# Performance work log

Measured on AMD Instinct MI355X. Metric: run time of the kernel, lower is better.

The kernel has to match this reference:

```python
import jax, jax.numpy as jnp
import numpy as np

N, D, W, S = 16384, 256, 64, 8  # utterances, embed dim, attention half-window, speakers


def setup_inputs() -> dict:
    key = jax.random.key(0)
    ks = jax.random.split(key, 8)
    scale = 1.0 / np.sqrt(D)
    return {
        "x": jax.random.normal(ks[0], (N, D), jnp.float32),
        "speaker_ids": jax.random.randint(ks[1], (N,), 0, S, jnp.int32),
        "W_att": jax.random.normal(ks[2], (D, D), jnp.float32) * scale,
        "W_pred": jax.random.normal(ks[3], (D, D), jnp.float32) * scale,
        "W_suc": jax.random.normal(ks[4], (D, D), jnp.float32) * scale,
        "W_same": jax.random.normal(ks[5], (D, D), jnp.float32) * scale,
        "W_diff": jax.random.normal(ks[6], (D, D), jnp.float32) * scale,
    }


def reference(x, speaker_ids, W_att, W_pred, W_suc, W_same, W_diff):
    n = x.shape[0]
    pad = jnp.zeros((W, D), x.dtype)
    # windowed gather: for utterance i, neighbors at offsets [-W, W-1] (2W slots)
    win_idx = jnp.arange(n)[:, None] + jnp.arange(2 * W)[None, :]  # index into padded [N+2W]
    xp = jnp.concatenate([pad, x, pad], axis=0)                    # [N+2W, D]
    windows = xp[win_idx]                                          # [N, 2W, D]
    # raw_attn[i,w] = (edge_att_weights(windows[i,w])) . x[i]
    raw_attn = jnp.einsum("nwd,ed,ne->nw", windows, W_att, x)      # [N, 2W]
    attn = jax.nn.softmax(raw_attn, axis=1)
    # relation masks over the band: j = i + offset
    offs = jnp.arange(2 * W) - W                                   # [-W, W-1]
    j = jnp.arange(n)[:, None] + offs[None, :]                     # [N, 2W]
    valid = (j >= 0) & (j < n)
    jc = jnp.clip(j, 0, n - 1)
    same_spk = speaker_ids[jc] == speaker_ids[:, None]
    masks = [
        valid & (offs >= 0)[None, :],   # pred: edges to current/future within window
        valid & (offs < 0)[None, :],    # suc: edges to past within window
        valid & same_spk,               # same speaker within window
        valid & ~same_spk,              # different speaker within window
    ]
    # relation-specific GCN aggregation: h = sum_r A_r @ (x @ W_r), A_r banded
    h = jnp.zeros_like(x)
    for Wr, m in zip([W_pred, W_suc, W_same, W_diff], masks):
        support = x @ Wr                                           # [N, D]
        sp = jnp.concatenate([pad, support, pad], axis=0)[win_idx]  # [N, 2W, D]
        h = h + jnp.einsum("nw,nwd->nd", attn * m, sp)
    return jax.nn.log_softmax(h, axis=1)
```

## Files before the change

### kernel.cpp

```cpp
#include <hip/hip_runtime.h>
#include <hip/hip_bf16.h>

typedef unsigned short u16;
typedef unsigned int u32;
typedef __attribute__((ext_vector_type(8))) short short8;
typedef __attribute__((ext_vector_type(4))) float floatx4;

#define NU 16384
#define DIM 256

#define XHo 0u
#define XLo 4194304u
#define XRo 8388608u
#define YHo 12582912u
#define YLo 16777216u
#define ST0 20971520u
#define STROW 16512u
#define STMAT 4227072u
#define WH0o 33652736u
#define WL0o 33718272u
#define WRo  33783808u

__device__ __forceinline__ u16 bfh(float v) {
  return (u16)(__float_as_uint(v) >> 16);
}
__device__ __forceinline__ float bup(u16 u) {
  return __uint_as_float(((u32)u) << 16);
}
__device__ __forceinline__ u16 bfrn(float v) {
  u32 u = __float_as_uint(v);
  return (u16)((u + 0x7fffu + ((u >> 16) & 1u)) >> 16);
}

__global__ __launch_bounds__(256) void xprep(const float* __restrict__ x,
                                             u16* __restrict__ ws) {
  int idx = (blockIdx.x * 256 + threadIdx.x) * 4;
  float4 v = *(const float4*)(x + idx);
  float a[4] = {v.x, v.y, v.z, v.w};
  u16 h[4], l[4], r[4];
#pragma unroll
  for (int q = 0; q < 4; ++q) {
    h[q] = bfh(a[q]);
    l[q] = bfh(a[q] - bup(h[q]));
    r[q] = bfrn(a[q]);
  }
  *(ushort4*)(ws + XHo + idx) = make_ushort4(h[0], h[1], h[2], h[3]);
  *(ushort4*)(ws + XLo + idx) = make_ushort4(l[0], l[1], l[2], l[3]);
  *(ushort4*)(ws + XRo + idx) = make_ushort4(r[0], r[1], r[2], r[3]);
}

__global__ __launch_bounds__(256) void wprep(
    const float* __restrict__ wat, const float* __restrict__ wpr,
    const float* __restrict__ wsu, const float* __restrict__ wsm,
    const float* __restrict__ wdf, u16* __restrict__ ws) {
  const int s = blockIdx.x, mat = blockIdx.y, n = threadIdx.x;
  const float* Wa = (mat == 0) ? wat : (mat == 1) ? wpr : (mat == 2) ? wsm : wsu;
  const float* Wb = (mat == 0) ? wat : (mat == 1) ? wsu : (mat == 2) ? wdf : wdf;
  const float c1  = (mat == 0) ? 0.f : (mat == 3) ? 1.f : -1.f;
  u16 hbuf[32], lbuf[32];
#pragma unroll 8
  for (int k = 0; k < 32; ++k) {
    float v = Wa[(s * 32 + k) * 256 + n] + c1 * Wb[(s * 32 + k) * 256 + n];
    if (mat == 0) { hbuf[k] = bfh(v); lbuf[k] = bfh(v - bup(hbuf[k])); }
    else          { hbuf[k] = bfrn(v); }
  }
  u16* dh = ws + ((mat == 0) ? WH0o : (WRo + (size_t)(mat - 1) * 65536))
             + (size_t)s * 8192 + n * 32;
#pragma unroll
  for (int p = 0; p < 4; ++p) *(uint4*)(dh + p * 8) = ((const uint4*)hbuf)[p];
  if (mat == 0) {
    u16* dl = ws + WL0o + (size_t)s * 8192 + n * 32;
#pragma unroll
    for (int p = 0; p < 4; ++p) *(uint4*)(dl + p * 8) = ((const uint4*)lbuf)[p];
  }
}

__global__ __launch_bounds__(256) void gzero(u16* __restrict__ ws) {
  int g = blockIdx.x * 256 + threadIdx.x;
  int r = g >> 13, rem = g & 8191;
  int d = rem >> 5, p = rem & 31;
  size_t base = ST0 + (size_t)r * STMAT + (size_t)d * STROW;
  size_t off = (p < 16) ? (base + p * 4) : (base + 16448 + (p - 16) * 4);
  *(ushort4*)(ws + off) = make_ushort4(0, 0, 0, 0);
}

__global__ __launch_bounds__(512) void gemmS(u16* __restrict__ ws) {
  __shared__ __align__(16) u16 Ahs[2048], Als[2048];
  __shared__ __align__(16) u16 BU[20480];

  const int t = threadIdx.x, mat = blockIdx.y, row0 = blockIdx.x * 64;
  const int w = t >> 6, ln = t & 15, quad = (t & 63) >> 4, q8 = quad * 8;
  const int n2base = w * 32;

  const u16* Wh = ws + ((mat == 0) ? WH0o : (WRo + (size_t)(mat - 1) * 65536));
  const u16* Wl = ws + WL0o;
  const u16* xh = ws + XHo;
  const u16* xl = ws + XLo;
  const u16* xr = ws + XRo;

  floatx4 acc[4][2];
#pragma unroll
  for (int m = 0; m < 4; ++m)
#pragma unroll
    for (int n2 = 0; n2 < 2; ++n2) acc[m][n2] = (floatx4){0.f, 0.f, 0.f, 0.f};

  for (int s = 0; s < 8; ++s) {
    if (mat == 0) {
      int c = t & 255, arow = c >> 2, apart = (c & 3) * 8;
      const u16* src = ((t < 256) ? xh : xl) + (size_t)(row0 + arow) * 256 + s * 32 + apart;
      u16* dst = ((t < 256) ? Ahs : Als) + arow * 32 + apart;
      *(uint4*)dst = *(const uint4*)src;
    } else if (t < 256) {
      int arow = t >> 2, apart = (t & 3) * 8;
      *(uint4*)(Ahs + arow * 32 + apart) =
          *(const uint4*)(xr + (size_t)(row0 + arow) * 256 + s * 32 + apart);
    }
    if (mat == 0) {
#pragma unroll
      for (int cc = 0; cc < 4; ++cc) {
        int c = t + 512 * cc;
        const u16* src = ((c < 1024) ? Wh : Wl) + (size_t)s * 8192 + (c & 1023) * 8;
        u16* dst = ((c < 1024) ? BU : BU + 8192) + (c & 1023) * 8;
        *(uint4*)dst = *(const uint4*)src;
      }
    } else {
#pragma unroll
      for (int cc = 0; cc < 2; ++cc) {
        int c = t + 512 * cc;
        *(uint4*)(BU + c * 8) = *(const uint4*)(Wh + (size_t)s * 8192 + c * 8);
      }
    }
    __syncthreads();

    short8 ah[4], al[4];
#pragma unroll
    for (int m = 0; m < 4; ++m) {
      ah[m] = *(const short8*)(Ahs + (m * 16 + ln) * 32 + q8);
      if (mat == 0) al[m] = *(const short8*)(Als + (m * 16 + ln) * 32 + q8);
    }
    short8 bh[2], bl[2];
#pragma unroll
    for (int n2 = 0; n2 < 2; ++n2) {
      int n = n2base + n2 * 16 + ln;
      bh[n2] = *(const short8*)(BU + n * 32 + q8);
      if (mat == 0) bl[n2] = *(const short8*)(BU + 8192 + n * 32 + q8);
    }
#pragma unroll
    for (int m = 0; m < 4; ++m)
#pragma unroll
      for (int n2 = 0; n2 < 2; ++n2) {
        acc[m][n2] = __builtin_amdgcn_mfma_f32_16x16x32_bf16(ah[m], bh[n2], acc[m][n2], 0, 0, 0);
        if (mat == 0) {
          acc[m][n2] = __builtin_amdgcn_mfma_f32_16x16x32_bf16(ah[m], bl[n2], acc[m][n2], 0, 0, 0);
          acc[m][n2] = __builtin_amdgcn_mfma_f32_16x16x32_bf16(al[m], bh[n2], acc[m][n2], 0, 0, 0);
        }
      }
    __syncthreads();
  }

  if (mat == 0) {
#pragma unroll
    for (int m = 0; m < 4; ++m)
#pragma unroll
      for (int n2 = 0; n2 < 2; ++n2) {
        int col = n2base + n2 * 16 + ln;
#pragma unroll
        for (int r = 0; r < 4; ++r) {
          int row = row0 + m * 16 + quad * 4 + r;
          float y = acc[m][n2][r];
          u16 hh = bfh(y);
          ws[YHo + (size_t)row * 256 + col] = hh;
          ws[YLo + (size_t)row * 256 + col] = bfh(y - bup(hh));
        }
      }
  } else {
#pragma unroll
    for (int m = 0; m < 4; ++m)
#pragma unroll
      for (int n2 = 0; n2 < 2; ++n2) {
        int col = n2base + n2 * 16 + ln;
        ushort4 pk = make_ushort4(bfrn(acc[m][n2][0]), bfrn(acc[m][n2][1]),
                                  bfrn(acc[m][n2][2]), bfrn(acc[m][n2][3]));
        *(ushort4*)(BU + col * 80 + m * 16 + quad * 4) = pk;
      }
    __syncthreads();
    u16* STm = ws + ST0 + (size_t)(mat - 1) * STMAT;
#pragma unroll
    for (int cc = 0; cc < 4; ++cc) {
      int c = t + 512 * cc;
      int d = c >> 3, part = c & 7;
      *(uint4*)(STm + (size_t)d * STROW + 64 + row0 + part * 8) =
          *(const uint4*)(BU + d * 80 + part * 8);
    }
  }
}

__global__ __launch_bounds__(512) void fused_attn(
    const u16* __restrict__ ws, const int* __restrict__ spk,
    float* __restrict__ out)
{
  __shared__ float Plds[64][196];
  __shared__ __align__(16) u16 stg[30720];
  __shared__ int spkw[192];
  __shared__ float pmax[64][8], psum[64][8], gmaxs[64], glse[64];

  const int t    = threadIdx.x;
  const int w    = t >> 6;
  const int ln   = t & 15;
  const int quad = (t & 63) >> 4;
  const int q8   = quad * 8;
  const int i0   = blockIdx.x * 64;

  if (t < 192) {
    int j = i0 + t - 64;
    spkw[t] = spk[min(max(j, 0), NU - 1)];
  }

  floatx4 accP[6];
#pragma unroll
  for (int cc = 0; cc < 6; ++cc) accP[cc] = (floatx4){0.f, 0.f, 0.f, 0.f};
  const int m0  = (w >> 1) * 16;
  const int ct0 = (w & 1) * 6;

  for (int kd = 0; kd < DIM; kd += 32) {
#pragma unroll
    for (int cc = 0; cc < 4; ++cc) {
      int c = t + 512 * cc;
      if (c < 1536) {
        int row = c >> 3, sub = c & 7, hil = sub >> 2, part = sub & 3;
        int jc = min(max(i0 + row - 64, 0), NU - 1);
        const u16* src = ws + (hil ? XLo : XHo) + (size_t)jc * 256 + kd + part * 8;
        *(uint4*)(stg + (hil ? 6144 : 0) + row * 32 + part * 8) = *(const uint4*)src;
      } else {
        int c2 = c - 1536;
        int row = c2 >> 3, sub = c2 & 7, hil = sub >> 2, part = sub & 3;
        const u16* src = ws + (hil ? YLo : YHo) + (size_t)(i0 + row) * 256 + kd + part * 8;
        *(uint4*)(stg + 12288 + (hil ? 2048 : 0) + row * 32 + part * 8) = *(const uint4*)src;
      }
    }
    __syncthreads();

    short8 ah = *(const short8*)(stg + 12288 + (m0 + ln) * 32 + q8);
    short8 al = *(const short8*)(stg + 14336 + (m0 + ln) * 32 + q8);
#pragma unroll
    for (int cc = 0; cc < 6; ++cc) {
      int xrow = (ct0 + cc) * 16 + ln;
      short8 bh = *(const short8*)(stg + xrow * 32 + q8);
      short8 bl = *(const short8*)(stg + 6144 + xrow * 32 + q8);
      accP[cc] = __builtin_amdgcn_mfma_f32_16x16x32_bf16(ah, bh, accP[cc], 0, 0, 0);
      accP[cc] = __builtin_amdgcn_mfma_f32_16x16x32_bf16(ah, bl, accP[cc], 0, 0, 0);
      accP[cc] = __builtin_amdgcn_mfma_f32_16x16x32_bf16(al, bh, accP[cc], 0, 0, 0);
    }
    __syncthreads();
  }
#pragma unroll
  for (int cc = 0; cc < 6; ++cc)
#pragma unroll
    for (int r = 0; r < 4; ++r)
      Plds[m0 + quad * 4 + r][(ct0 + cc) * 16 + ln] = accP[cc][r];
  __syncthreads();

  {
    int row = t >> 3, s = t & 7;
    float vals[16];
    float mx = -3.4e38f;
#pragma unroll
    for (int q = 0; q < 16; ++q) {
      int c = row + s * 16 + q;
      int j = i0 + c - 64;
      float pv = ((j >= 0) && (j < NU)) ? Plds[row][c] : 0.f;
      vals[q] = pv;
      mx = fmaxf(mx, pv);
    }
#pragma unroll
    for (int o = 1; o < 8; o <<= 1) mx = fmaxf(mx, __shfl_xor(mx, o));
    float sm = 0.f;
#pragma unroll
    for (int q = 0; q < 16; ++q) { vals[q] = __expf(vals[q] - mx); sm += vals[q]; }
#pragma unroll
    for (int o = 1; o < 8; o <<= 1) sm += __shfl_xor(sm, o);
    float inv = 1.f / sm;
#pragma unroll
    for (int q = 0; q < 16; ++q) {
      int c = row + s * 16 + q;
      int j = i0 + c - 64;
      Plds[row][c] = ((j >= 0) && (j < NU)) ? vals[q] * inv : 0.f;
    }
#pragma unroll
    for (int q = 0; q < 8; ++q) {
      int c2 = row + 128 + s * 8 + q;
      if (c2 >= 192) c2 -= 192;
      Plds[row][c2] = 0.f;
    }
  }
  __syncthreads();

  const int n0 = w * 32;
  floatx4 acc2[4][2];
#pragma unroll
  for (int m = 0; m < 4; ++m)
#pragma unroll
    for (int n2 = 0; n2 < 2; ++n2) acc2[m][n2] = (floatx4){0.f, 0.f, 0.f, 0.f};

  for (int kj = 0; kj < 192; kj += 32) {
    const int jcol = i0 + kj;
#pragma unroll
    for (int cc = 0; cc < 6; ++cc) {
      int c = t + 512 * cc;
      int r = c >> 10, d = (c >> 2) & 255, part = c & 3;
      const u16* src = ws + ST0 + (size_t)r * STMAT + (size_t)d * STROW + jcol + part * 8;
      *(uint4*)(stg + r * 8192 + d * 32 + part * 8) = *(const uint4*)src;
    }
    {
      int row = t >> 3, cg = t & 7, cb = kj + cg * 4;
      float4 av = *(const float4*)(&Plds[row][cb]);
      float aa[4] = {av.x, av.y, av.z, av.w};
      int sr = spkw[row + 64];
      u16 b0[4], b1[4], b2[4];
#pragma unroll
      for (int q = 0; q < 4; ++q) {
        int c = cb + q;
        u16 ab = bfrn(aa[q]);
        b0[q] = (c - row >= 64) ? ab : (u16)0;
        b1[q] = (spkw[c] == sr) ? ab : (u16)0;
        b2[q] = ab;
      }
      *(ushort4*)(stg + 24576 + row * 32 + cg * 4) = make_ushort4(b0[0], b0[1], b0[2], b0[3]);
      *(ushort4*)(stg + 26624 + row * 32 + cg * 4) = make_ushort4(b1[0], b1[1], b1[2], b1[3]);
      *(ushort4*)(stg + 28672 + row * 32 + cg * 4) = make_ushort4(b2[0], b2[1], b2[2], b2[3]);
    }
    __syncthreads();

    short8 af[3][4], bfv[3][2];
#pragma unroll
    for (int r = 0; r < 3; ++r) {
#pragma unroll
      for (int m = 0; m < 4; ++m)
        af[r][m] = *(const short8*)(stg + 24576 + r * 2048 + (m * 16 + ln) * 32 + q8);
#pragma unroll
      for (int n2 = 0; n2 < 2; ++n2) {
        int d = n0 + n2 * 16 + ln;
        bfv[r][n2] = *(const short8*)(stg + r * 8192 + d * 32 + q8);
      }
    }
#pragma unroll
    for (int r = 0; r < 3; ++r)
#pragma unroll
      for (int m = 0; m < 4; ++m)
#pragma unroll
        for (int n2 = 0; n2 < 2; ++n2)
          acc2[m][n2] = __builtin_amdgcn_mfma_f32_16x16x32_bf16(
              af[r][m], bfv[r][n2], acc2[m][n2], 0, 0, 0);
    __syncthreads();
  }

#pragma unroll
  for (int m = 0; m < 4; ++m)
#pragma unroll
    for (int r = 0; r < 4; ++r) {
      float v = fmaxf(acc2[m][0][r], acc2[m][1][r]);
#pragma unroll
      for (int o = 1; o < 16; o <<= 1) v = fmaxf(v, __shfl_xor(v, o));
      if (ln == 0) pmax[m * 16 + quad * 4 + r][w] = v;
    }
  __syncthreads();
  if (t < 64) {
    float g = pmax[t][0];
#pragma unroll
    for (int ww = 1; ww < 8; ++ww) g = fmaxf(g, pmax[t][ww]);
    gmaxs[t] = g;
  }
  __syncthreads();
#pragma unroll
  for (int m = 0; m < 4; ++m)
#pragma unroll
    for (int r = 0; r < 4; ++r) {
      float g = gmaxs[m * 16 + quad * 4 + r];
      float e = __expf(acc2[m][0][r] - g) + __expf(acc2[m][1][r] - g);
#pragma unroll
      for (int o = 1; o < 16; o <<= 1) e += __shfl_xor(e, o);
      if (ln == 0) psum[m * 16 + quad * 4 + r][w] = e;
    }
  __syncthreads();
  if (t < 64) {
    float s = psum[t][0];
#pragma unroll
    for (int ww = 1; ww < 8; ++ww) s += psum[t][ww];
    glse[t] = gmaxs[t] + logf(s);
  }
  __syncthreads();

#pragma unroll
  for (int m = 0; m < 4; ++m) {
    int rl0 = m * 16 + quad * 4;
#pragma unroll
    for (int r = 0; r < 4; ++r) {
      float l = glse[rl0 + r];
      size_t rowg = (size_t)(i0 + rl0 + r) * DIM;
      out[rowg + n0 + ln]      = acc2[m][0][r] - l;
      out[rowg + n0 + 16 + ln] = acc2[m][1][r] - l;
    }
  }
}

extern "C" void kernel_launch(void* const* d_in, const int* in_sizes, int n_in,
                              void* d_out, int out_size, void* d_ws, size_t ws_size,
                              hipStream_t stream) {
  const float* x   = (const float*)d_in[0];
  const int*   spk = (const int*)d_in[1];
  const float* wat = (const float*)d_in[2];
  const float* wpr = (const float*)d_in[3];
  const float* wsu = (const float*)d_in[4];
  const float* wsm = (const float*)d_in[5];
  const float* wdf = (const float*)d_in[6];
  float* out = (float*)d_out;
  u16* ws = (u16*)d_ws;

  hipLaunchKernelGGL(xprep, dim3(4096), dim3(256), 0, stream, x, ws);
  hipLaunchKernelGGL(wprep, dim3(8, 4), dim3(256), 0, stream,
                     wat, wpr, wsu, wsm, wdf, ws);
  hipLaunchKernelGGL(gzero, dim3(96), dim3(256), 0, stream, ws);
  hipLaunchKernelGGL(gemmS, dim3(256, 4), dim3(512), 0, stream, ws);
  hipLaunchKernelGGL(fused_attn, dim3(256), dim3(512), 0, stream, ws, spk, out);
}
```

Baseline: 169.0 us.

## Fuse attention projection into attn kernel and shrink tiles to 32 rows

Moves the x@W_att projection (three-pass split-bf16) out of gemmS and into fused_attn, so Y stays in LDS instead of round-tripping through global memory. The attention tile drops from 64 to 32 rows with a 160-column window, giving 512 blocks of 256 threads, and the X and ST operands are read straight from global memory instead of being staged through LDS. The weight-prep and zero-fill kernels are merged into one launch. In exchange, each block recomputes its own projection and depends on cache hits for the global reads that used to be staged.

```diff
diff --git a/kernel.cpp b/kernel.cpp
--- a/kernel.cpp
+++ b/kernel.cpp
@@ -8,18 +8,19 @@
 
 #define NU 16384
 #define DIM 256
+#define WIN 160
+#define YST 264
+#define AST 168
 
 #define XHo 0u
 #define XLo 4194304u
 #define XRo 8388608u
-#define YHo 12582912u
-#define YLo 16777216u
-#define ST0 20971520u
+#define ST0 12582912u
 #define STROW 16512u
 #define STMAT 4227072u
-#define WH0o 33652736u
-#define WL0o 33718272u
-#define WRo  33783808u
+#define WH0o 25264128u
+#define WL0o 25329664u
+#define WRo  25395200u
 
 __device__ __forceinline__ u16 bfh(float v) {
   return (u16)(__float_as_uint(v) >> 16);
@@ -49,53 +50,50 @@
   *(ushort4*)(ws + XRo + idx) = make_ushort4(r[0], r[1], r[2], r[3]);
 }
 
-__global__ __launch_bounds__(256) void wprep(
+__global__ __launch_bounds__(256) void wpgz(
     const float* __restrict__ wat, const float* __restrict__ wpr,
     const float* __restrict__ wsu, const float* __restrict__ wsm,
     const float* __restrict__ wdf, u16* __restrict__ ws) {
-  const int s = blockIdx.x, mat = blockIdx.y, n = threadIdx.x;
-  const float* Wa = (mat == 0) ? wat : (mat == 1) ? wpr : (mat == 2) ? wsm : wsu;
-  const float* Wb = (mat == 0) ? wat : (mat == 1) ? wsu : (mat == 2) ? wdf : wdf;
-  const float c1  = (mat == 0) ? 0.f : (mat == 3) ? 1.f : -1.f;
-  u16 hbuf[32], lbuf[32];
+  const int b = blockIdx.x, t = threadIdx.x;
+  if (b < 32) {
+    const int s = b & 7, mat = b >> 3, n = t;
+    const float* Wa = (mat == 0) ? wat : (mat == 1) ? wpr : (mat == 2) ? wsm : wsu;
+    const float* Wb = (mat == 0) ? wat : (mat == 1) ? wsu : (mat == 2) ? wdf : wdf;
+    const float c1  = (mat == 0) ? 0.f : (mat == 3) ? 1.f : -1.f;
+    u16 hbuf[32], lbuf[32];
 #pragma unroll 8
-  for (int k = 0; k < 32; ++k) {
-    float v = Wa[(s * 32 + k) * 256 + n] + c1 * Wb[(s * 32 + k) * 256 + n];
-    if (mat == 0) { hbuf[k] = bfh(v); lbuf[k] = bfh(v - bup(hbuf[k])); }
-    else          { hbuf[k] = bfrn(v); }
-  }
-  u16* dh = ws + ((mat == 0) ? WH0o : (WRo + (size_t)(mat - 1) * 65536))
-             + (size_t)s * 8192 + n * 32;
-#pragma unroll
-  for (int p = 0; p < 4; ++p) *(uint4*)(dh + p * 8) = ((const uint4*)hbuf)[p];
-  if (mat == 0) {
-    u16* dl = ws + WL0o + (size_t)s * 8192 + n * 32;
-#pragma unroll
-    for (int p = 0; p < 4; ++p) *(uint4*)(dl + p * 8) = ((const uint4*)lbuf)[p];
-  }
-}
-
-__global__ __launch_bounds__(256) void gzero(u16* __restrict__ ws) {
-  int g = blockIdx.x * 256 + threadIdx.x;
-  int r = g >> 13, rem = g & 8191;
-  int d = rem >> 5, p = rem & 31;
-  size_t base = ST0 + (size_t)r * STMAT + (size_t)d * STROW;
-  size_t off = (p < 16) ? (base + p * 4) : (base + 16448 + (p - 16) * 4);
-  *(ushort4*)(ws + off) = make_ushort4(0, 0, 0, 0);
+    for (int k = 0; k < 32; ++k) {
+      float v = Wa[(s * 32 + k) * 256 + n] + c1 * Wb[(s * 32 + k) * 256 + n];
+      if (mat == 0) { hbuf[k] = bfh(v); lbuf[k] = bfh(v - bup(hbuf[k])); }
+      else          { hbuf[k] = bfrn(v); }
+    }
+    u16* dh = ws + ((mat == 0) ? WH0o : (WRo + (size_t)(mat - 1) * 65536))
+               + (size_t)s * 8192 + n * 32;
+#pragma unroll
+    for (int p = 0; p < 4; ++p) *(uint4*)(dh + p * 8) = ((const uint4*)hbuf)[p];
+    if (mat == 0) {
+      u16* dl = ws + WL0o + (size_t)s * 8192 + n * 32;
+#pragma unroll
+      for (int p = 0; p < 4; ++p) *(uint4*)(dl + p * 8) = ((const uint4*)lbuf)[p];
+    }
+  } else {
+    int g = (b - 32) * 256 + t;
+    int r = g >> 13, rem = g & 8191;
+    int d = rem >> 5, p = rem & 31;
+    size_t base = ST0 + (size_t)r * STMAT + (size_t)d * STROW;
+    size_t off = (p < 16) ? (base + p * 4) : (base + 16448 + (p - 16) * 4);
+    *(ushort4*)(ws + off) = make_ushort4(0, 0, 0, 0);
+  }
 }
 
 __global__ __launch_bounds__(512) void gemmS(u16* __restrict__ ws) {
-  __shared__ __align__(16) u16 Ahs[2048], Als[2048];
+  __shared__ __align__(16) u16 Ahs[2048];
   __shared__ __align__(16) u16 BU[20480];
 
-  const int t = threadIdx.x, mat = blockIdx.y, row0 = blockIdx.x * 64;
+  const int t = threadIdx.x, row0 = blockIdx.x * 64;
   const int w = t >> 6, ln = t & 15, quad = (t & 63) >> 4, q8 = quad * 8;
   const int n2base = w * 32;
-
-  const u16* Wh = ws + ((mat == 0) ? WH0o : (WRo + (size_t)(mat - 1) * 65536));
-  const u16* Wl = ws + WL0o;
-  const u16* xh = ws + XHo;
-  const u16* xl = ws + XLo;
+  const u16* Wh = ws + WRo + (size_t)blockIdx.y * 65536;
   const u16* xr = ws + XRo;
 
   floatx4 acc[4][2];
@@ -105,302 +103,273 @@
     for (int n2 = 0; n2 < 2; ++n2) acc[m][n2] = (floatx4){0.f, 0.f, 0.f, 0.f};
 
   for (int s = 0; s < 8; ++s) {
-    if (mat == 0) {
-      int c = t & 255, arow = c >> 2, apart = (c & 3) * 8;
-      const u16* src = ((t < 256) ? xh : xl) + (size_t)(row0 + arow) * 256 + s * 32 + apart;
-      u16* dst = ((t < 256) ? Ahs : Als) + arow * 32 + apart;
-      *(uint4*)dst = *(const uint4*)src;
-    } else if (t < 256) {
+    if (t < 256) {
       int arow = t >> 2, apart = (t & 3) * 8;
       *(uint4*)(Ahs + arow * 32 + apart) =
           *(const uint4*)(xr + (size_t)(row0 + arow) * 256 + s * 32 + apart);
     }
-    if (mat == 0) {
-#pragma unroll
-      for (int cc = 0; cc < 4; ++cc) {
-        int c = t + 512 * cc;
-        const u16* src = ((c < 1024) ? Wh : Wl) + (size_t)s * 8192 + (c & 1023) * 8;
-        u16* dst = ((c < 1024) ? BU : BU + 8192) + (c & 1023) * 8;
-        *(uint4*)dst = *(const uint4*)src;
-      }
-    } else {
-#pragma unroll
-      for (int cc = 0; cc < 2; ++cc) {
-        int c = t + 512 * cc;
-        *(uint4*)(BU + c * 8) = *(const uint4*)(Wh + (size_t)s * 8192 + c * 8);
-      }
+#pragma unroll
+    for (int cc = 0; cc < 2; ++cc) {
+      int c = t + 512 * cc;
+      *(uint4*)(BU + c * 8) = *(const uint4*)(Wh + (size_t)s * 8192 + c * 8);
     }
     __syncthreads();
 
-    short8 ah[4], al[4];
-#pragma unroll
-    for (int m = 0; m < 4; ++m) {
+    short8 ah[4];
+#pragma unroll
+    for (int m = 0; m < 4; ++m)
       ah[m] = *(const short8*)(Ahs + (m * 16 + ln) * 32 + q8);
-      if (mat == 0) al[m] = *(const short8*)(Als + (m * 16 + ln) * 32 + q8);
-    }
-    short8 bh[2], bl[2];
+    short8 bh[2];
+#pragma unroll
+    for (int n2 = 0; n2 < 2; ++n2)
+      bh[n2] = *(const short8*)(BU + (n2base + n2 * 16 + ln) * 32 + q8);
+#pragma unroll
+    for (int m = 0; m < 4; ++m)
+#pragma unroll
+      for (int n2 = 0; n2 < 2; ++n2)
+        acc[m][n2] = __builtin_amdgcn_mfma_f32_16x16x32_bf16(ah[m], bh[n2], acc[m][n2], 0, 0, 0);
+    __syncthreads();
+  }
+
+#pragma unroll
+  for (int m = 0; m < 4; ++m)
 #pragma unroll
     for (int n2 = 0; n2 < 2; ++n2) {
-      int n = n2base + n2 * 16 + ln;
-      bh[n2] = *(const short8*)(BU + n * 32 + q8);
-      if (mat == 0) bl[n2] = *(const short8*)(BU + 8192 + n * 32 + q8);
-    }
-#pragma unroll
-    for (int m = 0; m < 4; ++m)
-#pragma unroll
-      for (int n2 = 0; n2 < 2; ++n2) {
-        acc[m][n2] = __builtin_amdgcn_mfma_f32_16x16x32_bf16(ah[m], bh[n2], acc[m][n2], 0, 0, 0);
-        if (mat == 0) {
-          acc[m][n2] = __builtin_amdgcn_mfma_f32_16x16x32_bf16(ah[m], bl[n2], acc[m][n2], 0, 0, 0);
-          acc[m][n2] = __builtin_amdgcn_mfma_f32_16x16x32_bf16(al[m], bh[n2], acc[m][n2], 0, 0, 0);
-        }
-      }
-    __syncthreads();
-  }
-
-  if (mat == 0) {
-#pragma unroll
-    for (int m = 0; m < 4; ++m)
-#pragma unroll
-      for (int n2 = 0; n2 < 2; ++n2) {
-        int col = n2base + n2 * 16 + ln;
-#pragma unroll
-        for (int r = 0; r < 4; ++r) {
-          int row = row0 + m * 16 + quad * 4 + r;
-          float y = acc[m][n2][r];
-          u16 hh = bfh(y);
-          ws[YHo + (size_t)row * 256 + col] = hh;
-          ws[YLo + (size_t)row * 256 + col] = bfh(y - bup(hh));
-        }
-      }
-  } else {
-#pragma unroll
-    for (int m = 0; m < 4; ++m)
-#pragma unroll
-      for (int n2 = 0; n2 < 2; ++n2) {
-        int col = n2base + n2 * 16 + ln;
-        ushort4 pk = make_ushort4(bfrn(acc[m][n2][0]), bfrn(acc[m][n2][1]),
-                                  bfrn(acc[m][n2][2]), bfrn(acc[m][n2][3]));
-        *(ushort4*)(BU + col * 80 + m * 16 + quad * 4) = pk;
-      }
-    __syncthreads();
-    u16* STm = ws + ST0 + (size_t)(mat - 1) * STMAT;
-#pragma unroll
-    for (int cc = 0; cc < 4; ++cc) {
-      int c = t + 512 * cc;
-      int d = c >> 3, part = c & 7;
-      *(uint4*)(STm + (size_t)d * STROW + 64 + row0 + part * 8) =
-          *(const uint4*)(BU + d * 80 + part * 8);
-    }
-  }
-}
-
-__global__ __launch_bounds__(512) void fused_attn(
+      int col = n2base + n2 * 16 + ln;
+      ushort4 pk = make_ushort4(bfrn(acc[m][n2][0]), bfrn(acc[m][n2][1]),
+                                bfrn(acc[m][n2][2]), bfrn(acc[m][n2][3]));
+      *(ushort4*)(BU + col * 80 + m * 16 + quad * 4) = pk;
+    }
+  __syncthreads();
+  u16* STm = ws + ST0 + (size_t)blockIdx.y * STMAT;
+#pragma unroll
+  for (int cc = 0; cc < 4; ++cc) {
+    int c = t + 512 * cc;
+    int d = c >> 3, part = c & 7;
+    *(uint4*)(STm + (size_t)d * STROW + 64 + row0 + part * 8) =
+        *(const uint4*)(BU + d * 80 + part * 8);
+  }
+}
+
+__global__ __launch_bounds__(256) void fused_attn(
     const u16* __restrict__ ws, const int* __restrict__ spk,
     float* __restrict__ out)
 {
-  __shared__ float Plds[64][196];
-  __shared__ __align__(16) u16 stg[30720];
-  __shared__ int spkw[192];
-  __shared__ float pmax[64][8], psum[64][8], gmaxs[64], glse[64];
+  __shared__ __align__(16) u16 Yh[32 * YST], Yl[32 * YST];
+  __shared__ __align__(16) u16 Am[3 * 32 * AST];
+  __shared__ float prt[32][4];
+  __shared__ float lsx[32][4];
+  __shared__ int spkw[WIN];
 
   const int t    = threadIdx.x;
   const int w    = t >> 6;
   const int ln   = t & 15;
   const int quad = (t & 63) >> 4;
   const int q8   = quad * 8;
-  const int i0   = blockIdx.x * 64;
-
-  if (t < 192) {
-    int j = i0 + t - 64;
-    spkw[t] = spk[min(max(j, 0), NU - 1)];
-  }
-
-  floatx4 accP[6];
-#pragma unroll
-  for (int cc = 0; cc < 6; ++cc) accP[cc] = (floatx4){0.f, 0.f, 0.f, 0.f};
-  const int m0  = (w >> 1) * 16;
-  const int ct0 = (w & 1) * 6;
+  const int i0   = blockIdx.x * 32;
+
+  if (t < WIN) spkw[t] = spk[min(max(i0 - 64 + t, 0), NU - 1)];
+
+  const int n0 = w * 64;
+  floatx4 acc0[2][4];
+#pragma unroll
+  for (int m = 0; m < 2; ++m)
+#pragma unroll
+    for (int nt = 0; nt < 4; ++nt) acc0[m][nt] = (floatx4){0.f, 0.f, 0.f, 0.f};
+
+  for (int s = 0; s < 8; ++s) {
+    short8 ah[2], al[2];
+#pragma unroll
+    for (int m = 0; m < 2; ++m) {
+      size_t ro = (size_t)(i0 + m * 16 + ln) * DIM + s * 32 + q8;
+      ah[m] = *(const short8*)(ws + XHo + ro);
+      al[m] = *(const short8*)(ws + XLo + ro);
+    }
+    short8 bh[4], bl[4];
+#pragma unroll
+    for (int nt = 0; nt < 4; ++nt) {
+      size_t bo = (size_t)s * 8192 + (n0 + nt * 16 + ln) * 32 + q8;
+      bh[nt] = *(const short8*)(ws + WH0o + bo);
+      bl[nt] = *(const short8*)(ws + WL0o + bo);
+    }
+#pragma unroll
+    for (int m = 0; m < 2; ++m)
+#pragma unroll
+      for (int nt = 0; nt < 4; ++nt) {
+        acc0[m][nt] = __builtin_amdgcn_mfma_f32_16x16x32_bf16(ah[m], bh[nt], acc0[m][nt], 0, 0, 0);
+        acc0[m][nt] = __builtin_amdgcn_mfma_f32_16x16x32_bf16(ah[m], bl[nt], acc0[m][nt], 0, 0, 0);
+        acc0[m][nt] = __builtin_amdgcn_mfma_f32_16x16x32_bf16(al[m], bh[nt], acc0[m][nt], 0, 0, 0);
+      }
+  }
+#pragma unroll
+  for (int m = 0; m < 2; ++m)
+#pragma unroll
+    for (int nt = 0; nt < 4; ++nt) {
+      int col = n0 + nt * 16 + ln;
+#pragma unroll
+      for (int r = 0; r < 4; ++r) {
+        int row = m * 16 + quad * 4 + r;
+        float y = acc0[m][nt][r];
+        u16 hh = bfh(y);
+        Yh[row * YST + col] = hh;
+        Yl[row * YST + col] = bfh(y - bup(hh));
+      }
+    }
+  __syncthreads();
+
+  const int mrow = w & 1;
+  const int ct0  = (w >> 1) * 5;
+  const int half = w >> 1;
+  floatx4 acc1[5];
+#pragma unroll
+  for (int cc = 0; cc < 5; ++cc) acc1[cc] = (floatx4){0.f, 0.f, 0.f, 0.f};
 
   for (int kd = 0; kd < DIM; kd += 32) {
-#pragma unroll
-    for (int cc = 0; cc < 4; ++cc) {
-      int c = t + 512 * cc;
-      if (c < 1536) {
-        int row = c >> 3, sub = c & 7, hil = sub >> 2, part = sub & 3;
-        int jc = min(max(i0 + row - 64, 0), NU - 1);
-        const u16* src = ws + (hil ? XLo : XHo) + (size_t)jc * 256 + kd + part * 8;
-        *(uint4*)(stg + (hil ? 6144 : 0) + row * 32 + part * 8) = *(const uint4*)src;
-      } else {
-        int c2 = c - 1536;
-        int row = c2 >> 3, sub = c2 & 7, hil = sub >> 2, part = sub & 3;
-        const u16* src = ws + (hil ? YLo : YHo) + (size_t)(i0 + row) * 256 + kd + part * 8;
-        *(uint4*)(stg + 12288 + (hil ? 2048 : 0) + row * 32 + part * 8) = *(const uint4*)src;
+    short8 yh8 = *(const short8*)(Yh + (mrow * 16 + ln) * YST + kd + q8);
+    short8 yl8 = *(const short8*)(Yl + (mrow * 16 + ln) * YST + kd + q8);
+#pragma unroll
+    for (int cc = 0; cc < 5; ++cc) {
+      int j  = i0 - 64 + (ct0 + cc) * 16 + ln;
+      int jc = min(max(j, 0), NU - 1);
+      size_t xo = (size_t)jc * DIM + kd + q8;
+      short8 xbh = *(const short8*)(ws + XHo + xo);
+      short8 xbl = *(const short8*)(ws + XLo + xo);
+      acc1[cc] = __builtin_amdgcn_mfma_f32_16x16x32_bf16(yh8, xbh, acc1[cc], 0, 0, 0);
+      acc1[cc] = __builtin_amdgcn_mfma_f32_16x16x32_bf16(yh8, xbl, acc1[cc], 0, 0, 0);
+      acc1[cc] = __builtin_amdgcn_mfma_f32_16x16x32_bf16(yl8, xbh, acc1[cc], 0, 0, 0);
+    }
+  }
+
+  int  c_of[5];
+  bool vj[5];
+#pragma unroll
+  for (int cc = 0; cc < 5; ++cc) {
+    c_of[cc] = (ct0 + cc) * 16 + ln;
+    int j = i0 - 64 + c_of[cc];
+    vj[cc] = (j >= 0) && (j < NU);
+  }
+#pragma unroll
+  for (int r = 0; r < 4; ++r) {
+    int row = mrow * 16 + quad * 4 + r;
+    float mx = -3.4e38f;
+#pragma unroll
+    for (int cc = 0; cc < 5; ++cc) {
+      int rel = c_of[cc] - row;
+      bool inb = (rel >= 0) && (rel < 128);
+      float v = inb ? (vj[cc] ? acc1[cc][r] : 0.f) : -3.4e38f;
+      mx = fmaxf(mx, v);
+    }
+#pragma unroll
+    for (int o = 1; o < 16; o <<= 1) mx = fmaxf(mx, __shfl_xor(mx, o));
+    if (ln == 0) prt[row][half] = mx;
+  }
+  __syncthreads();
+  float gmax[4], gsum[4];
+#pragma unroll
+  for (int r = 0; r < 4; ++r) {
+    int row = mrow * 16 + quad * 4 + r;
+    float gm = fmaxf(prt[row][0], prt[row][1]);
+    gmax[r] = gm;
+    float s = 0.f;
+#pragma unroll
+    for (int cc = 0; cc < 5; ++cc) {
+      int rel = c_of[cc] - row;
+      bool inb = (rel >= 0) && (rel < 128);
+      float vv = vj[cc] ? acc1[cc][r] : 0.f;
+      float e  = inb ? __expf(vv - gm) : 0.f;
+      s += e;
+      acc1[cc][r] = (inb && vj[cc]) ? e : 0.f;
+    }
+#pragma unroll
+    for (int o = 1; o < 16; o <<= 1) s += __shfl_xor(s, o);
+    if (ln == 0) prt[row][2 + half] = s;
+  }
+  __syncthreads();
+#pragma unroll
+  for (int r = 0; r < 4; ++r) {
+    int row = mrow * 16 + quad * 4 + r;
+    gsum[r] = prt[row][2] + prt[row][3];
+  }
+#pragma unroll
+  for (int r = 0; r < 4; ++r) {
+    int row = mrow * 16 + quad * 4 + r;
+    float inv = 1.f / gsum[r];
+    int myspk = spkw[row + 64];
+#pragma unroll
+    for (int cc = 0; cc < 5; ++cc) {
+      int c = c_of[cc];
+      u16 ab = bfrn(acc1[cc][r] * inv);
+      Am[(0 * 32 + row) * AST + c] = (c - row >= 64) ? ab : (u16)0;
+      Am[(1 * 32 + row) * AST + c] = (spkw[c] == myspk) ? ab : (u16)0;
+      Am[(2 * 32 + row) * AST + c] = ab;
+    }
+  }
+  __syncthreads();
+
+  floatx4 acc2[2][4];
+#pragma unroll
+  for (int m = 0; m < 2; ++m)
+#pragma unroll
+    for (int nt = 0; nt < 4; ++nt) acc2[m][nt] = (floatx4){0.f, 0.f, 0.f, 0.f};
+
+  for (int kj = 0; kj < WIN; kj += 32) {
+#pragma unroll
+    for (int rel = 0; rel < 3; ++rel) {
+      short8 af[2];
+#pragma unroll
+      for (int m = 0; m < 2; ++m)
+        af[m] = *(const short8*)(Am + (rel * 32 + m * 16 + ln) * AST + kj + q8);
+#pragma unroll
+      for (int nt = 0; nt < 4; ++nt) {
+        size_t so = (size_t)ST0 + (size_t)rel * STMAT
+                  + (size_t)(n0 + nt * 16 + ln) * STROW + (i0 + kj) + q8;
+        short8 bf8 = *(const short8*)(ws + so);
+#pragma unroll
+        for (int m = 0; m < 2; ++m)
+          acc2[m][nt] = __builtin_amdgcn_mfma_f32_16x16x32_bf16(af[m], bf8, acc2[m][nt], 0, 0, 0);
       }
     }
-    __syncthreads();
-
-    short8 ah = *(const short8*)(stg + 12288 + (m0 + ln) * 32 + q8);
-    short8 al = *(const short8*)(stg + 14336 + (m0 + ln) * 32 + q8);
-#pragma unroll
-    for (int cc = 0; cc < 6; ++cc) {
-      int xrow = (ct0 + cc) * 16 + ln;
-      short8 bh = *(const short8*)(stg + xrow * 32 + q8);
-      short8 bl = *(const short8*)(stg + 6144 + xrow * 32 + q8);
-      accP[cc] = __builtin_amdgcn_mfma_f32_16x16x32_bf16(ah, bh, accP[cc], 0, 0, 0);
-      accP[cc] = __builtin_amdgcn_mfma_f32_16x16x32_bf16(ah, bl, accP[cc], 0, 0, 0);
-      accP[cc] = __builtin_amdgcn_mfma_f32_16x16x32_bf16(al, bh, accP[cc], 0, 0, 0);
-    }
-    __syncthreads();
-  }
-#pragma unroll
-  for (int cc = 0; cc < 6; ++cc)
-#pragma unroll
-    for (int r = 0; r < 4; ++r)
-      Plds[m0 + quad * 4 + r][(ct0 + cc) * 16 + ln] = accP[cc][r];
-  __syncthreads();
-
-  {
-    int row = t >> 3, s = t & 7;
-    float vals[16];
-    float mx = -3.4e38f;
-#pragma unroll
-    for (int q = 0; q < 16; ++q) {
-      int c = row + s * 16 + q;
-      int j = i0 + c - 64;
-      float pv = ((j >= 0) && (j < NU)) ? Plds[row][c] : 0.f;
-      vals[q] = pv;
-      mx = fmaxf(mx, pv);
-    }
-#pragma unroll
-    for (int o = 1; o < 8; o <<= 1) mx = fmaxf(mx, __shfl_xor(mx, o));
-    float sm = 0.f;
-#pragma unroll
-    for (int q = 0; q < 16; ++q) { vals[q] = __expf(vals[q] - mx); sm += vals[q]; }
-#pragma unroll
-    for (int o = 1; o < 8; o <<= 1) sm += __shfl_xor(sm, o);
-    float inv = 1.f / sm;
-#pragma unroll
-    for (int q = 0; q < 16; ++q) {
-      int c = row + s * 16 + q;
-      int j = i0 + c - 64;
-      Plds[row][c] = ((j >= 0) && (j < NU)) ? vals[q] * inv : 0.f;
-    }
-#pragma unroll
-    for (int q = 0; q < 8; ++q) {
-      int c2 = row + 128 + s * 8 + q;
-      if (c2 >= 192) c2 -= 192;
-      Plds[row][c2] = 0.f;
-    }
-  }
-  __syncthreads();
-
-  const int n0 = w * 32;
-  floatx4 acc2[4][2];
-#pragma unroll
-  for (int m = 0; m < 4; ++m)
-#pragma unroll
-    for (int n2 = 0; n2 < 2; ++n2) acc2[m][n2] = (floatx4){0.f, 0.f, 0.f, 0.f};
-
-  for (int kj = 0; kj < 192; kj += 32) {
-    const int jcol = i0 + kj;
-#pragma unroll
-    for (int cc = 0; cc < 6; ++cc) {
-      int c = t + 512 * cc;
-      int r = c >> 10, d = (c >> 2) & 255, part = c & 3;
-      const u16* src = ws + ST0 + (size_t)r * STMAT + (size_t)d * STROW + jcol + part * 8;
-      *(uint4*)(stg + r * 8192 + d * 32 + part * 8) = *(const uint4*)src;
-    }
-    {
-      int row = t >> 3, cg = t & 7, cb = kj + cg * 4;
-      float4 av = *(const float4*)(&Plds[row][cb]);
-      float aa[4] = {av.x, av.y, av.z, av.w};
-      int sr = spkw[row + 64];
-      u16 b0[4], b1[4], b2[4];
-#pragma unroll
-      for (int q = 0; q < 4; ++q) {
-        int c = cb + q;
-        u16 ab = bfrn(aa[q]);
-        b0[q] = (c - row >= 64) ? ab : (u16)0;
-        b1[q] = (spkw[c] == sr) ? ab : (u16)0;
-        b2[q] = ab;
-      }
-      *(ushort4*)(stg + 24576 + row * 32 + cg * 4) = make_ushort4(b0[0], b0[1], b0[2], b0[3]);
-      *(ushort4*)(stg + 26624 + row * 32 + cg * 4) = make_ushort4(b1[0], b1[1], b1[2], b1[3]);
-      *(ushort4*)(stg + 28672 + row * 32 + cg * 4) = make_ushort4(b2[0], b2[1], b2[2], b2[3]);
-    }
-    __syncthreads();
-
-    short8 af[3][4], bfv[3][2];
-#pragma unroll
-    for (int r = 0; r < 3; ++r) {
-#pragma unroll
-      for (int m = 0; m < 4; ++m)
-        af[r][m] = *(const short8*)(stg + 24576 + r * 2048 + (m * 16 + ln) * 32 + q8);
-#pragma unroll
-      for (int n2 = 0; n2 < 2; ++n2) {
-        int d = n0 + n2 * 16 + ln;
-        bfv[r][n2] = *(const short8*)(stg + r * 8192 + d * 32 + q8);
-      }
-    }
-#pragma unroll
-    for (int r = 0; r < 3; ++r)
-#pragma unroll
-      for (int m = 0; m < 4; ++m)
-#pragma unroll
-        for (int n2 = 0; n2 < 2; ++n2)
-          acc2[m][n2] = __builtin_amdgcn_mfma_f32_16x16x32_bf16(
-              af[r][m], bfv[r][n2], acc2[m][n2], 0, 0, 0);
-    __syncthreads();
-  }
-
-#pragma unroll
-  for (int m = 0; m < 4; ++m)
+  }
+
+#pragma unroll
+  for (int m = 0; m < 2; ++m)
 #pragma unroll
     for (int r = 0; r < 4; ++r) {
-      float v = fmaxf(acc2[m][0][r], acc2[m][1][r]);
+      float v = fmaxf(fmaxf(acc2[m][0][r], acc2[m][1][r]),
+                      fmaxf(acc2[m][2][r], acc2[m][3][r]));
 #pragma unroll
       for (int o = 1; o < 16; o <<= 1) v = fmaxf(v, __shfl_xor(v, o));
-      if (ln == 0) pmax[m * 16 + quad * 4 + r][w] = v;
-    }
-  __syncthreads();
-  if (t < 64) {
-    float g = pmax[t][0];
-#pragma unroll
-    for (int ww = 1; ww < 8; ++ww) g = fmaxf(g, pmax[t][ww]);
-    gmaxs[t] = g;
-  }
-  __syncthreads();
-#pragma unroll
-  for (int m = 0; m < 4; ++m)
+      if (ln == 0) lsx[m * 16 + quad * 4 + r][w] = v;
+    }
+  __syncthreads();
+#pragma unroll
+  for (int m = 0; m < 2; ++m)
 #pragma unroll
     for (int r = 0; r < 4; ++r) {
-      float g = gmaxs[m * 16 + quad * 4 + r];
-      float e = __expf(acc2[m][0][r] - g) + __expf(acc2[m][1][r] - g);
+      int row = m * 16 + quad * 4 + r;
+      float g = fmaxf(fmaxf(lsx[row][0], lsx[row][1]),
+                      fmaxf(lsx[row][2], lsx[row][3]));
+      float e = 0.f;
+#pragma unroll
+      for (int nt = 0; nt < 4; ++nt) e += __expf(acc2[m][nt][r] - g);
 #pragma unroll
       for (int o = 1; o < 16; o <<= 1) e += __shfl_xor(e, o);
-      if (ln == 0) psum[m * 16 + quad * 4 + r][w] = e;
-    }
-  __syncthreads();
-  if (t < 64) {
-    float s = psum[t][0];
-#pragma unroll
-    for (int ww = 1; ww < 8; ++ww) s += psum[t][ww];
-    glse[t] = gmaxs[t] + logf(s);
-  }
-  __syncthreads();
-
-#pragma unroll
-  for (int m = 0; m < 4; ++m) {
-    int rl0 = m * 16 + quad * 4;
+      if (ln == 0) prt[row][w] = e;
+    }
+  __syncthreads();
+#pragma unroll
+  for (int m = 0; m < 2; ++m)
 #pragma unroll
     for (int r = 0; r < 4; ++r) {
-      float l = glse[rl0 + r];
-      size_t rowg = (size_t)(i0 + rl0 + r) * DIM;
-      out[rowg + n0 + ln]      = acc2[m][0][r] - l;
-      out[rowg + n0 + 16 + ln] = acc2[m][1][r] - l;
-    }
-  }
+      int row = m * 16 + quad * 4 + r;
+      float g = fmaxf(fmaxf(lsx[row][0], lsx[row][1]),
+                      fmaxf(lsx[row][2], lsx[row][3]));
+      float lse = g + logf(prt[row][0] + prt[row][1] + prt[row][2] + prt[row][3]);
+      size_t rowg = (size_t)(i0 + row) * DIM;
+#pragma unroll
+      for (int nt = 0; nt < 4; ++nt)
+        out[rowg + n0 + nt * 16 + ln] = acc2[m][nt][r] - lse;
+    }
 }
 
 extern "C" void kernel_launch(void* const* d_in, const int* in_sizes, int n_in,
@@ -417,9 +386,8 @@
   u16* ws = (u16*)d_ws;
 
   hipLaunchKernelGGL(xprep, dim3(4096), dim3(256), 0, stream, x, ws);
-  hipLaunchKernelGGL(wprep, dim3(8, 4), dim3(256), 0, stream,
+  hipLaunchKernelGGL(wpgz, dim3(128), dim3(256), 0, stream,
                      wat, wpr, wsu, wsm, wdf, ws);
-  hipLaunchKernelGGL(gzero, dim3(96), dim3(256), 0, stream, ws);
-  hipLaunchKernelGGL(gemmS, dim3(256, 4), dim3(512), 0, stream, ws);
-  hipLaunchKernelGGL(fused_attn, dim3(256), dim3(512), 0, stream, ws, spk, out);
-}
+  hipLaunchKernelGGL(gemmS, dim3(256, 3), dim3(512), 0, stream, ws);
+  hipLaunchKernelGGL(fused_attn, dim3(512), dim3(256), 0, stream, ws, spk, out);
+}
```

After: 196.5 us. +16.2%, slower.
